# Optimization experiments

Hardware: AMD Instinct MI355X
Metric: run time of the kernel (lower is better)

The kernel has to match this reference:

```python
import jax, jax.numpy as jnp
import numpy as np

B, N, ND, H = 8, 1024, 64, 128
NUM_OPS, NUM_PARAMS, SKETCH = 64, 256, 128


def setup_inputs() -> dict:
    key = jax.random.key(0)
    ks = iter(jax.random.split(key, 64))

    def rn(shape, s=0.05):
        return jax.random.normal(next(ks), shape, dtype=jnp.float32) * s

    inp = {
        'node_features': jax.random.normal(next(ks), (B, N, ND), dtype=jnp.float32),
        'adjacency': (jax.random.uniform(next(ks), (B, N, N)) < 0.05).astype(jnp.float32),
        'mask': jnp.ones((B, N), jnp.float32),
    }
    for name, din in (('g1', ND), ('g2', H), ('g3', H)):
        inp[name + '_W'] = rn((din, H))
        inp[name + '_b'] = jnp.zeros((H,), jnp.float32)
        inp[name + '_aW'] = rn((2 * H,))
        inp[name + '_ab'] = jnp.zeros((), jnp.float32)
    for l in (0, 1):
        inp[f'l{l}_Wih'] = rn((4 * H, H))
        inp[f'l{l}_Whh'] = rn((4 * H, H))
        inp[f'l{l}_bih'] = jnp.zeros((4 * H,), jnp.float32)
        inp[f'l{l}_bhh'] = jnp.zeros((4 * H,), jnp.float32)
    for name, dout in (('op', NUM_OPS), ('pa', NUM_PARAMS), ('sk', SKETCH), ('no', ND)):
        inp[name + '_W1'] = rn((H, H))
        inp[name + '_b1'] = jnp.zeros((H,), jnp.float32)
        inp[name + '_W2'] = rn((H, dout))
        inp[name + '_b2'] = jnp.zeros((dout,), jnp.float32)
    return inp


def _gnn(x, adj, W, b, aW, ab):
    # h = Linear(x); att[b,i,j] = sigmoid(aW . [h_j ; h_i] + ab)  (cat order from the torch code)
    h = x @ W + b                      # [B,N,H]
    D = W.shape[1]
    sj = h @ aW[:D]                    # contribution of the dim-1-expanded term (h_j)
    si = h @ aW[D:]                    # contribution of the dim-2-expanded term (h_i)
    att = jax.nn.sigmoid(si[:, :, None] + sj[:, None, :] + ab) * adj  # [B,N,N]
    return jnp.einsum('bij,bjd->bid', att, h)


def _lstm(x, Wih, Whh, bih, bhh):
    # single torch-style LSTM layer, gate order i,f,g,o; zero initial state
    Bx, Hh = x.shape[0], Whh.shape[1]

    def step(carry, xt):
        h, c = carry
        g = xt @ Wih.T + h @ Whh.T + (bih + bhh)       # [B,4H]
        i, f, gg, o = jnp.split(g, 4, axis=-1)
        c = jax.nn.sigmoid(f) * c + jax.nn.sigmoid(i) * jnp.tanh(gg)
        h = jax.nn.sigmoid(o) * jnp.tanh(c)
        return (h, c), h

    z = jnp.zeros((Bx, Hh), x.dtype)
    _, ys = jax.lax.scan(step, (z, z), jnp.swapaxes(x, 0, 1))
    return jnp.swapaxes(ys, 0, 1)


def _mlp(x, W1, b1, W2, b2):
    return jax.nn.relu(x @ W1 + b1) @ W2 + b2


def reference(node_features, adjacency, mask,
              g1_W, g1_b, g1_aW, g1_ab,
              g2_W, g2_b, g2_aW, g2_ab,
              g3_W, g3_b, g3_aW, g3_ab,
              l0_Wih, l0_Whh, l0_bih, l0_bhh,
              l1_Wih, l1_Whh, l1_bih, l1_bhh,
              op_W1, op_b1, op_W2, op_b2,
              pa_W1, pa_b1, pa_W2, pa_b2,
              sk_W1, sk_b1, sk_W2, sk_b2,
              no_W1, no_b1, no_W2, no_b2):
    h = jax.nn.relu(_gnn(node_features, adjacency, g1_W, g1_b, g1_aW, g1_ab))
    h = jax.nn.relu(_gnn(h, adjacency, g2_W, g2_b, g2_aW, g2_ab))
    h = _gnn(h, adjacency, g3_W, g3_b, g3_aW, g3_ab)
    lo = _lstm(h, l0_Wih, l0_Whh, l0_bih, l0_bhh)
    lo = _lstm(lo, l1_Wih, l1_Whh, l1_bih, l1_bhh)
    op_pred = _mlp(lo, op_W1, op_b1, op_W2, op_b2)
    param_pred = _mlp(lo, pa_W1, pa_b1, pa_W2, pa_b2)
    sketch_pred = _mlp(lo, sk_W1, sk_b1, sk_W2, sk_b2)
    node_pred = _mlp(h, no_W1, no_b1, no_W2, no_b2)
    return (op_pred, param_pred, sketch_pred, node_pred)
```

## Files before the change

### kernel.cpp

```cpp
#include <hip/hip_runtime.h>

typedef __attribute__((ext_vector_type(8))) short short8;
typedef __attribute__((ext_vector_type(4))) float f32x4;
typedef __attribute__((ext_vector_type(2))) float f32x2;
typedef __attribute__((ext_vector_type(4))) unsigned short us4;
typedef __attribute__((ext_vector_type(2))) unsigned int u32x2;

__device__ __forceinline__ unsigned short bf16_of(float f) {
    unsigned u = __builtin_bit_cast(unsigned, f);
    u += 0x7fffu + ((u >> 16) & 1u);
    return (unsigned short)(u >> 16);
}
__device__ __forceinline__ unsigned bf16pk(float a, float b) {
    return (unsigned)bf16_of(a) | ((unsigned)bf16_of(b) << 16);
}
__device__ __forceinline__ float fexp2(float x) { return __builtin_amdgcn_exp2f(x); }
__device__ __forceinline__ float frcp(float x) { return __builtin_amdgcn_rcpf(x); }
__device__ __forceinline__ float sigm(float x) { return frcp(1.f + fexp2(-1.44269504f * x)); }
__device__ __forceinline__ float tanh_f(float x) {
    float e = fexp2(2.88539008f * x);
    return 1.f - 2.f * frcp(e + 1.f);
}
__device__ __forceinline__ f32x4 mfma16(short8 a, short8 b, f32x4 c) {
    return __builtin_amdgcn_mfma_f32_16x16x32_bf16(a, b, c, 0, 0, 0);
}
__device__ __forceinline__ float dpp_shr8(float x) {
    return __builtin_bit_cast(float, __builtin_amdgcn_update_dpp(
        0, __builtin_bit_cast(int, x), 0x118, 0xF, 0xF, true));
}
__device__ __forceinline__ float dpp_shl8(float x) {
    return __builtin_bit_cast(float, __builtin_amdgcn_update_dpp(
        0, __builtin_bit_cast(int, x), 0x108, 0xF, 0xF, true));
}

__global__ __launch_bounds__(256) void gemm_f32(
    const float* __restrict__ A, const float* __restrict__ B,
    const float* __restrict__ bias, float* __restrict__ C,
    int M, int N, int K, int BT, int RELU, int PACK)
{
    __shared__ float As[64][33];
    __shared__ float Bs[32][68];
    const int tid = threadIdx.x;
    const int tx = tid & 15, ty = tid >> 4;
    const int m0 = blockIdx.y * 64, n0 = blockIdx.x * 64;
    float acc[4][4];
#pragma unroll
    for (int i = 0; i < 4; ++i)
#pragma unroll
        for (int j = 0; j < 4; ++j) acc[i][j] = 0.f;

    for (int k0 = 0; k0 < K; k0 += 32) {
        __syncthreads();
        {
            const int r = tid >> 2, kk = (tid & 3) * 8;
            const float* src = A + (size_t)(m0 + r) * K + k0 + kk;
            f32x4 v0 = *(const f32x4*)src;
            f32x4 v1 = *(const f32x4*)(src + 4);
#pragma unroll
            for (int e = 0; e < 4; ++e) { As[r][kk + e] = v0[e]; As[r][kk + 4 + e] = v1[e]; }
        }
        if (!BT) {
            const int kk = tid >> 3, nn = (tid & 7) * 8;
            const float* src = B + (size_t)(k0 + kk) * N + n0 + nn;
            f32x4 v0 = *(const f32x4*)src;
            f32x4 v1 = *(const f32x4*)(src + 4);
#pragma unroll
            for (int e = 0; e < 4; ++e) { Bs[kk][nn + e] = v0[e]; Bs[kk][nn + 4 + e] = v1[e]; }
        } else {
            const int n = tid >> 2, kk = (tid & 3) * 8;
            const float* src = B + (size_t)(n0 + n) * K + k0 + kk;
            f32x4 v0 = *(const f32x4*)src;
            f32x4 v1 = *(const f32x4*)(src + 4);
#pragma unroll
            for (int e = 0; e < 4; ++e) { Bs[kk + e][n] = v0[e]; Bs[kk + 4 + e][n] = v1[e]; }
        }
        __syncthreads();
#pragma unroll 8
        for (int k = 0; k < 32; ++k) {
            float a0 = As[ty * 4 + 0][k], a1 = As[ty * 4 + 1][k];
            float a2 = As[ty * 4 + 2][k], a3 = As[ty * 4 + 3][k];
            f32x4 bv = *(const f32x4*)&Bs[k][tx * 4];
#pragma unroll
            for (int j = 0; j < 4; ++j) {
                acc[0][j] += a0 * bv[j]; acc[1][j] += a1 * bv[j];
                acc[2][j] += a2 * bv[j]; acc[3][j] += a3 * bv[j];
            }
        }
    }
    f32x4 bv = {};
    if (bias != nullptr) bv = *(const f32x4*)&bias[n0 + tx * 4];
#pragma unroll
    for (int i = 0; i < 4; ++i) {
        f32x4 res = {};
#pragma unroll
        for (int j = 0; j < 4; ++j) {
            float v = acc[i][j] + bv[j];
            if (RELU) v = fmaxf(v, 0.f);
            res[j] = v;
        }
        const int m = m0 + ty * 4 + i;
        if (!PACK) {
            *(f32x4*)&C[(size_t)m * N + n0 + tx * 4] = res;
        } else {
            const int b = m >> 10, t = m & 1023;
            const int n = n0 + tx * 4;
            const int pr = n >> 7, h = n & 127;
            *(f32x4*)&C[(((size_t)t * 4 + pr) * 8 + b) * 128 + h] = res;
        }
    }
}

__global__ __launch_bounds__(256) void sisj_kernel(
    const float* __restrict__ h, const float* __restrict__ aW,
    float* __restrict__ si, float* __restrict__ sj)
{
    const int tid = threadIdx.x, lane = tid & 63, w = tid >> 6;
    const int row = blockIdx.x * 4 + w;
    f32x2 hv = *(const f32x2*)(h + (size_t)row * 128 + lane * 2);
    f32x2 w1 = *(const f32x2*)&aW[lane * 2];
    f32x2 w2 = *(const f32x2*)&aW[128 + lane * 2];
    float sjp = hv[0] * w1[0] + hv[1] * w1[1];
    float sip = hv[0] * w2[0] + hv[1] * w2[1];
#pragma unroll
    for (int o = 32; o > 0; o >>= 1) {
        sjp += __shfl_xor(sjp, o);
        sip += __shfl_xor(sip, o);
    }
    if (lane == 0) { si[row] = sip; sj[row] = sjp; }
}

__global__ __launch_bounds__(256) void transpose_bf16_k(
    const float* __restrict__ h, unsigned short* __restrict__ hT)
{
    __shared__ float t[64][65];
    const int b = blockIdx.z, jt = blockIdx.x, dt = blockIdx.y;
    const int tid = threadIdx.x;
    const int r = tid >> 4, c4 = (tid & 15) * 4;
#pragma unroll
    for (int rr = 0; rr < 4; ++rr) {
        const int j = rr * 16 + r;
        f32x4 v = *(const f32x4*)(h + ((size_t)b * 1024 + jt * 64 + j) * 128 + dt * 64 + c4);
#pragma unroll
        for (int e = 0; e < 4; ++e) t[j][c4 + e] = v[e];
    }
    __syncthreads();
#pragma unroll
    for (int rr = 0; rr < 4; ++rr) {
        const int d = rr * 16 + r;
        u32x2 o;
        o[0] = bf16pk(t[c4 + 0][d], t[c4 + 1][d]);
        o[1] = bf16pk(t[c4 + 2][d], t[c4 + 3][d]);
        *(u32x2*)(hT + ((size_t)b * 128 + dt * 64 + d) * 1024 + jt * 64 + c4) = o;
    }
}

__global__ __launch_bounds__(256) void gnn_agg(
    const float* __restrict__ adj, const unsigned short* __restrict__ hT,
    const float* __restrict__ si, const float* __restrict__ sj,
    const float* __restrict__ abp, float* __restrict__ out, int RELU)
{
    __shared__ __align__(16) unsigned short Alds[64 * 40];
    __shared__ __align__(16) unsigned short Blds[128 * 40];
    const int b = blockIdx.y, it = blockIdx.x;
    const int i0 = it * 64;
    const int tid = threadIdx.x, lane = tid & 63, w = tid >> 6;
    const int quad = lane >> 4, col = lane & 15;
    const float ab = abp[0];
    const float* adjb = adj + (size_t)b * 1024 * 1024;
    const unsigned short* hTb = hT + (size_t)b * 128 * 1024;
    const float* sjb = sj + b * 1024;

    f32x4 acc[8] = {};
    const int ar_ = tid >> 2, ash = (tid & 3) * 8;
    const int br_ = tid >> 1, bsh = (tid & 1) * 16;
    const float sii = si[b * 1024 + i0 + ar_] + ab;

    for (int j0 = 0; j0 < 1024; j0 += 32) {
        __syncthreads();
        {
            const float* ar = adjb + (size_t)(i0 + ar_) * 1024 + j0 + ash;
            f32x4 av0 = *(const f32x4*)ar;
            f32x4 av1 = *(const f32x4*)(ar + 4);
            float s[8];
#pragma unroll
            for (int e = 0; e < 4; ++e) {
                s[e]     = sigm(sii + sjb[j0 + ash + e])     * av0[e];
                s[4 + e] = sigm(sii + sjb[j0 + ash + 4 + e]) * av1[e];
            }
            u32x2 o0 = {bf16pk(s[0], s[1]), bf16pk(s[2], s[3])};
            u32x2 o1 = {bf16pk(s[4], s[5]), bf16pk(s[6], s[7])};
            unsigned short* al = Alds + ar_ * 40 + ash;
            *(u32x2*)&al[0] = o0;
            *(u32x2*)&al[4] = o1;
        }
        {
            const unsigned short* bsrc = hTb + (size_t)br_ * 1024 + j0 + bsh;
            unsigned short* bl = Blds + br_ * 40 + bsh;
            *(short8*)&bl[0] = *(const short8*)&bsrc[0];
            *(short8*)&bl[8] = *(const short8*)&bsrc[8];
        }
        __syncthreads();
        short8 af = *(const short8*)&Alds[(w * 16 + col) * 40 + quad * 8];
#pragma unroll
        for (int nt = 0; nt < 8; ++nt) {
            short8 bf = *(const short8*)&Blds[(nt * 16 + col) * 40 + quad * 8];
            acc[nt] = mfma16(af, bf, acc[nt]);
        }
    }
    const int ibase = i0 + w * 16 + quad * 4;
#pragma unroll
    for (int nt = 0; nt < 8; ++nt) {
        const int d = nt * 16 + col;
#pragma unroll
        for (int r = 0; r < 4; ++r) {
            float v = acc[nt][r];
            if (RELU) v = fmaxf(v, 0.f);
            out[((size_t)b * 1024 + ibase + r) * 128 + d] = v;
        }
    }
}

struct PrepArgs {
    const float* src[8];
    unsigned short* dst[8];
    int N[8];
};
__global__ __launch_bounds__(256) void prep_k(
    PrepArgs pa, const float* bih0, const float* bhh0,
    float* bsum, int* flags)
{
    const int m = blockIdx.x;
    const int tid = threadIdx.x;
    if (m < 8) {
        const float* src = pa.src[m];
        unsigned short* dst = pa.dst[m];
        const int N = pa.N[m];
        const int n0 = tid >> 4, kc = (tid & 15) * 8;
        for (int n = n0; n < N; n += 16) {
            unsigned o[4];
#pragma unroll
            for (int e = 0; e < 8; e += 2)
                o[e >> 1] = bf16pk(src[(size_t)(kc + e) * N + n],
                                   src[(size_t)(kc + e + 1) * N + n]);
            *(u32x2*)&dst[n * 128 + kc] = *(u32x2*)&o[0];
            *(u32x2*)&dst[n * 128 + kc + 4] = *(u32x2*)&o[2];
        }
    } else {
        bsum[tid] = bih0[tid] + bhh0[tid];
        bsum[tid + 256] = bih0[tid + 256] + bhh0[tid + 256];
        if (tid < 3) flags[tid] = 0;
    }
}


struct HeadArgs {
    const unsigned short* W1T[4];
    const float* b1[4];
    const unsigned short* W2T[4];
    const float* b2[4];
    float* outp[4];
};

__device__ __forceinline__ void lstm_epilogue(
    const f32x4 accs[4], f32x4 xv0, f32x4 xv1, float* cst, float* hv, bool lo)
{
    float t0[4], t1[4];
#pragma unroll
    for (int i = 0; i < 4; ++i) {
        float P0 = 0.5f * ((lo ? accs[0][i] : dpp_shr8(accs[1][i])) + xv0[i]);
        float P1r = (lo ? accs[2][i] : dpp_shr8(accs[3][i])) + xv1[i];
        float P1 = lo ? P1r : 0.5f * P1r;
        t0[i] = tanh_f(P0);
        t1[i] = tanh_f(P1);
    }
    float c2[4], og[4];
#pragma unroll
    for (int i = 0; i < 4; ++i) {
        float ig = 0.5f + 0.5f * t0[i];
        float fg = 0.5f + 0.5f * dpp_shl8(t0[i]);
        float gg = t1[i];
        og[i] = 0.5f + 0.5f * dpp_shl8(t1[i]);
        c2[i] = fg * cst[i] + ig * gg;
        cst[i] = c2[i];
    }
    float pc0 = lo ? c2[0] : dpp_shr8(c2[1]);
    float pc1 = lo ? c2[2] : dpp_shr8(c2[3]);
    float tc0 = tanh_f(pc0), tc1 = tanh_f(pc1);
    float th[4] = {tc0, dpp_shl8(tc0), tc1, dpp_shl8(tc1)};
#pragma unroll
    for (int i = 0; i < 4; ++i) hv[i] = og[i] * th[i];
}

template <int SINK>
__device__ __forceinline__ void lstm_step(
    unsigned short* Hc, unsigned short* Hn, const short8 afr[4][4],
    f32x4 xv0, f32x4 xv1, float* cst, unsigned short* __restrict__ sink,
    int t, int col, int quad, int h4, int b)
{
    short8 bfr[4];
#pragma unroll
    for (int c = 0; c < 4; ++c)
        bfr[c] = *(const short8*)&Hc[col * 136 + c * 32 + quad * 8];
    f32x4 accs[4] = {};
#pragma unroll
    for (int c = 0; c < 4; ++c)
#pragma unroll
        for (int g = 0; g < 4; ++g)
            accs[g] = mfma16(afr[g][c], bfr[c], accs[g]);

    const bool lo = (col < 8);
    float hv[4];
    lstm_epilogue(accs, xv0, xv1, cst, hv, lo);
    if (lo) {
        u32x2 hb = {bf16pk(hv[0], hv[1]), bf16pk(hv[2], hv[3])};
        *(u32x2*)&Hn[b * 136 + h4] = hb;
        if (SINK == 0)
            *(u32x2*)(sink + (size_t)t * 1024 + b * 128 + h4) = hb;
        else
            *(u32x2*)(sink + ((size_t)t * 8 + b) * 128 + h4) = hb;
    }
    __builtin_amdgcn_s_waitcnt(0xC07F);
    __builtin_amdgcn_s_barrier();
}

template <int A32, int LROWS>
__device__ void head_strip(
    const void* __restrict__ Asrc, int row0,
    const unsigned short* __restrict__ W1T, const float* __restrict__ b1,
    const unsigned short* __restrict__ W2T, const float* __restrict__ b2,
    float* __restrict__ outp, int dout, unsigned short* A2, int tid)
{
    const int lane = tid & 63, w = tid >> 6;
    const int quad = lane >> 4, col = lane & 15;
    const int mrow = w * 16 + col;
    f32x4 acc[8] = {};
#pragma unroll
    for (int kc = 0; kc < 4; ++kc) {
        short8 af;
        if (A32) {
            const float* s = (const float*)Asrc + (size_t)(row0 + mrow) * 128 + kc * 32 + quad * 8;
            f32x4 v0 = *(const f32x4*)s, v1 = *(const f32x4*)(s + 4);
            short8 v;
#pragma unroll
            for (int j = 0; j < 4; ++j) {
                v[j] = (short)bf16_of(v0[j]);
                v[4 + j] = (short)bf16_of(v1[j]);
            }
            af = v;
        } else {
            af = *(const short8*)((const unsigned short*)Asrc +
                                  (size_t)(row0 + mrow) * 128 + kc * 32 + quad * 8);
        }
#pragma unroll
        for (int nt = 0; nt < 8; ++nt) {
            short8 bf = *(const short8*)&W1T[(nt * 16 + col) * 128 + kc * 32 + quad * 8];
            acc[nt] = mfma16(af, bf, acc[nt]);
        }
    }
    float b1v[8];
#pragma unroll
    for (int nt = 0; nt < 8; ++nt) b1v[nt] = b1[nt * 16 + col];
    __syncthreads();
#pragma unroll
    for (int nt = 0; nt < 8; ++nt)
#pragma unroll
        for (int i = 0; i < 4; ++i) {
            const int mm = w * 16 + quad * 4 + i;
            A2[mm * 136 + nt * 16 + col] = bf16_of(fmaxf(acc[nt][i] + b1v[nt], 0.f));
        }
    __syncthreads();
    const int ntiles = dout >> 4;
    for (int np = 0; np < ntiles; np += 8) {
        const int nts = (ntiles - np < 8) ? ntiles - np : 8;
        f32x4 acc2[8] = {};
#pragma unroll
        for (int kc = 0; kc < 4; ++kc) {
            short8 a2f = *(const short8*)&A2[mrow * 136 + kc * 32 + quad * 8];
            for (int nt = 0; nt < nts; ++nt) {
                short8 bf = *(const short8*)&W2T[((np + nt) * 16 + col) * 128 + kc * 32 + quad * 8];
                acc2[nt] = mfma16(a2f, bf, acc2[nt]);
            }
        }
        for (int nt = 0; nt < nts; ++nt) {
            const int n = (np + nt) * 16 + col;
            const float bb = b2[n];
#pragma unroll
            for (int i = 0; i < 4; ++i) {
                const int r = row0 + w * 16 + quad * 4 + i;
                size_t off;
                if (LROWS) off = ((size_t)(r & 7) * 1024 + (r >> 3)) * dout + n;
                else       off = (size_t)r * dout + n;
                outp[off] = acc2[nt][i] + bb;
            }
        }
    }
}

__global__ __launch_bounds__(512) void lstm_pipe(
    const float* __restrict__ xw0, const float* __restrict__ Whh0,
    const float* __restrict__ Wih1, const float* __restrict__ Whh1,
    const float* __restrict__ bih1, const float* __restrict__ bhh1,
    unsigned short* __restrict__ hbuf, float* __restrict__ xw1,
    int* __restrict__ flags, unsigned short* __restrict__ out1b,
    const float* __restrict__ bufH3, HeadArgs ha)
{
    __shared__ __align__(16) unsigned short H[2][16 * 136];
    __shared__ __align__(16) unsigned short A2[128 * 136];
    const int tid = threadIdx.x;
    const int lane = tid & 63;
    const int w = tid >> 6;
    const int quad = lane >> 4;
    const int col = lane & 15;
    const int b = col & 7;
    const int prA = col >> 3;
    const int h4 = w * 16 + quad * 4;

    if (blockIdx.x >= 3) {
        const int wid = blockIdx.x - 3;
        for (int s = wid; s < 64; s += 8)
            head_strip<1, 0>(bufH3, s * 128, ha.W1T[3], ha.b1[3],
                             ha.W2T[3], ha.b2[3], ha.outp[3], 64, A2, tid);
        for (int s = wid; s < 64; s += 8) {
            if (tid == 0) {
                while (__hip_atomic_load(&flags[2], __ATOMIC_ACQUIRE,
                                         __HIP_MEMORY_SCOPE_AGENT) < s + 1)
                    __builtin_amdgcn_s_sleep(16);
            }
            __syncthreads();
            head_strip<0, 1>(out1b, s * 128, ha.W1T[0], ha.b1[0],
                             ha.W2T[0], ha.b2[0], ha.outp[0], 64, A2, tid);
            head_strip<0, 1>(out1b, s * 128, ha.W1T[1], ha.b1[1],
                             ha.W2T[1], ha.b2[1], ha.outp[1], 256, A2, tid);
            head_strip<0, 1>(out1b, s * 128, ha.W1T[2], ha.b1[2],
                             ha.W2T[2], ha.b2[2], ha.outp[2], 128, A2, tid);
        }
        return;
    }

    if (blockIdx.x == 1) {
        short8 afrI[4][4];
        f32x4 biasv[4];
#pragma unroll
        for (int g = 0; g < 4; ++g) {
            const int row = g * 128 + w * 16 + col;
#pragma unroll
            for (int c = 0; c < 4; ++c) {
                const float* src = Wih1 + row * 128 + c * 32 + quad * 8;
                short8 v;
#pragma unroll
                for (int j = 0; j < 8; ++j) v[j] = (short)bf16_of(src[j]);
                afrI[g][c] = v;
            }
            const int rb = g * 128 + w * 16 + quad * 4;
            f32x4 b1 = *(const f32x4*)&bih1[rb];
            f32x4 b2 = *(const f32x4*)&bhh1[rb];
#pragma unroll
            for (int e = 0; e < 4; ++e) biasv[g][e] = b1[e] + b2[e];
        }
        for (int k = 0; k < 64; ++k) {
            if (tid == 0) {
                while (__hip_atomic_load(&flags[0], __ATOMIC_ACQUIRE,
                                         __HIP_MEMORY_SCOPE_AGENT) < k + 1)
                    __builtin_amdgcn_s_sleep(2);
                if (k >= 4) {
                    while (__hip_atomic_load(&flags[2], __ATOMIC_RELAXED,
                                             __HIP_MEMORY_SCOPE_AGENT) < k - 3)
                        __builtin_amdgcn_s_sleep(2);
                }
            }
            __builtin_amdgcn_s_waitcnt(0xC07F);
            __builtin_amdgcn_s_barrier();
            const unsigned short* hb = hbuf + (size_t)k * 16 * 1024;
            float* dst = xw1 + (size_t)(k & 3) * 65536;
#pragma unroll 2
            for (int nt = 0; nt < 8; ++nt) {
                const int tl = nt * 2 + (col >> 3);
                const unsigned short* src = hb + tl * 1024 + b * 128 + quad * 8;
                short8 bfr[4];
#pragma unroll
                for (int c = 0; c < 4; ++c) bfr[c] = *(const short8*)&src[c * 32];
                f32x4 acc[4] = {};
#pragma unroll
                for (int c = 0; c < 4; ++c)
#pragma unroll
                    for (int g = 0; g < 4; ++g)
                        acc[g] = mfma16(afrI[g][c], bfr[c], acc[g]);
#pragma unroll
                for (int g = 0; g < 4; ++g) {
                    f32x4 res;
#pragma unroll
                    for (int e = 0; e < 4; ++e) res[e] = acc[g][e] + biasv[g][e];
                    *(f32x4*)&dst[((tl * 4 + g) * 8 + b) * 128 + w * 16 + quad * 4] = res;
                }
            }
            __builtin_amdgcn_s_waitcnt(0x0F70);
            __builtin_amdgcn_s_barrier();
            if (tid == 0)
                __hip_atomic_store(&flags[1], k + 1, __ATOMIC_RELEASE,
                                   __HIP_MEMORY_SCOPE_AGENT);
        }
        return;
    }

    for (int i = tid; i < 2 * 16 * 136; i += 512) (&H[0][0])[i] = 0;
    float cst[4] = {0.f, 0.f, 0.f, 0.f};
    const int lane_off = (prA * 8 + b) * 128 + h4;

    if (blockIdx.x == 0) {
        short8 afr[4][4];
#pragma unroll
        for (int g = 0; g < 4; ++g) {
            const int row = g * 128 + w * 16 + col;
#pragma unroll
            for (int c = 0; c < 4; ++c) {
                const float* src = Whh0 + row * 128 + c * 32 + quad * 8;
                short8 v;
#pragma unroll
                for (int j = 0; j < 8; ++j) v[j] = (short)bf16_of(src[j]);
                afr[g][c] = v;
            }
        }
        const float* xp = xw0 + lane_off;
        f32x4 p0a = *(const f32x4*)(xp);
        f32x4 p1a = *(const f32x4*)(xp + 2048);
        f32x4 p0b = *(const f32x4*)(xp + 4096);
        f32x4 p1b = *(const f32x4*)(xp + 6144);
        xp += 8192;
        __syncthreads();

        for (int t = 0; t < 1024; t += 2) {
            const float* xr = (t == 1022) ? xp - 8192 : xp;
            {
                f32x4 xv0 = p0a, xv1 = p1a;
                p0a = *(const f32x4*)(xr);
                p1a = *(const f32x4*)(xr + 2048);
                lstm_step<0>(&H[0][0], &H[1][0], afr, xv0, xv1, cst, hbuf, t, col, quad, h4, b);
            }
            {
                f32x4 xv0 = p0b, xv1 = p1b;
                p0b = *(const f32x4*)(xr + 4096);
                p1b = *(const f32x4*)(xr + 6144);
                lstm_step<0>(&H[1][0], &H[0][0], afr, xv0, xv1, cst, hbuf, t + 1, col, quad, h4, b);
            }
            xp += 8192;
            if ((t & 14) == 14) {
                __syncthreads();
                if (tid == 0)
                    __hip_atomic_store(&flags[0], (t >> 4) + 1, __ATOMIC_RELEASE,
                                       __HIP_MEMORY_SCOPE_AGENT);
            }
        }
    } else {
        short8 afr[4][4];
#pragma unroll
        for (int g = 0; g < 4; ++g) {
            const int row = g * 128 + w * 16 + col;
#pragma unroll
            for (int c = 0; c < 4; ++c) {
                const float* src = Whh1 + row * 128 + c * 32 + quad * 8;
                short8 v;
#pragma unroll
                for (int j = 0; j < 8; ++j) v[j] = (short)bf16_of(src[j]);
                afr[g][c] = v;
            }
        }
        __syncthreads();
        auto xaddr = [&](int t) -> const float* {
            return xw1 + (((t >> 4) & 3) * 65536 + (t & 15) * 4096) + lane_off;
        };
        while (__hip_atomic_load(&flags[1], __ATOMIC_ACQUIRE,
                                 __HIP_MEMORY_SCOPE_AGENT) < 2)
            __builtin_amdgcn_s_sleep(2);
        f32x4 p0a = *(const f32x4*)xaddr(0);
        f32x4 p1a = *(const f32x4*)(xaddr(0) + 2048);
        f32x4 p0b = *(const f32x4*)xaddr(1);
        f32x4 p1b = *(const f32x4*)(xaddr(1) + 2048);

        for (int c = 0; c < 64; ++c) {
            if (c > 0) {
                const int target = (c + 2 < 64) ? c + 2 : 64;
                if (tid == 0) {
                    while (__hip_atomic_load(&flags[1], __ATOMIC_ACQUIRE,
                                             __HIP_MEMORY_SCOPE_AGENT) < target)
                        __builtin_amdgcn_s_sleep(2);
                }
                __builtin_amdgcn_s_waitcnt(0xC07F);
                __builtin_amdgcn_s_barrier();
            }
            for (int s = 0; s < 16; s += 2) {
                const int t = c * 16 + s;
                const int t2 = (t + 2 < 1024) ? t + 2 : 1023;
                const int t3 = (t + 3 < 1024) ? t + 3 : 1023;
                {
                    f32x4 xv0 = p0a, xv1 = p1a;
                    p0a = *(const f32x4*)xaddr(t2);
                    p1a = *(const f32x4*)(xaddr(t2) + 2048);
                    lstm_step<1>(&H[0][0], &H[1][0], afr, xv0, xv1, cst, out1b, t, col, quad, h4, b);
                }
                {
                    f32x4 xv0 = p0b, xv1 = p1b;
                    p0b = *(const f32x4*)xaddr(t3);
                    p1b = *(const f32x4*)(xaddr(t3) + 2048);
                    lstm_step<1>(&H[1][0], &H[0][0], afr, xv0, xv1, cst, out1b, t + 1, col, quad, h4, b);
                }
            }
            __syncthreads();
            if (tid == 0)
                __hip_atomic_store(&flags[2], c + 1, __ATOMIC_RELEASE,
                                   __HIP_MEMORY_SCOPE_AGENT);
        }
    }
}

extern "C" void kernel_launch(void* const* d_in, const int* in_sizes, int n_in,
                              void* d_out, int out_size, void* d_ws, size_t ws_size,
                              hipStream_t stream)
{
    (void)in_sizes; (void)n_in; (void)out_size; (void)ws_size;
    const float* nf    = (const float*)d_in[0];
    const float* adj   = (const float*)d_in[1];
    const float* g1W   = (const float*)d_in[3];
    const float* g1b   = (const float*)d_in[4];
    const float* g1aW  = (const float*)d_in[5];
    const float* g1ab  = (const float*)d_in[6];
    const float* g2W   = (const float*)d_in[7];
    const float* g2b   = (const float*)d_in[8];
    const float* g2aW  = (const float*)d_in[9];
    const float* g2ab  = (const float*)d_in[10];
    const float* g3W   = (const float*)d_in[11];
    const float* g3b   = (const float*)d_in[12];
    const float* g3aW  = (const float*)d_in[13];
    const float* g3ab  = (const float*)d_in[14];
    const float* l0Wih = (const float*)d_in[15];
    const float* l0Whh = (const float*)d_in[16];
    const float* l0bih = (const float*)d_in[17];
    const float* l0bhh = (const float*)d_in[18];
    const float* l1Wih = (const float*)d_in[19];
    const float* l1Whh = (const float*)d_in[20];
    const float* l1bih = (const float*)d_in[21];
    const float* l1bhh = (const float*)d_in[22];
    const float* opW1 = (const float*)d_in[23];
    const float* opb1 = (const float*)d_in[24];
    const float* opW2 = (const float*)d_in[25];
    const float* opb2 = (const float*)d_in[26];
    const float* paW1 = (const float*)d_in[27];
    const float* pab1 = (const float*)d_in[28];
    const float* paW2 = (const float*)d_in[29];
    const float* pab2 = (const float*)d_in[30];
    const float* skW1 = (const float*)d_in[31];
    const float* skb1 = (const float*)d_in[32];
    const float* skW2 = (const float*)d_in[33];
    const float* skb2 = (const float*)d_in[34];
    const float* noW1 = (const float*)d_in[35];
    const float* nob1 = (const float*)d_in[36];
    const float* noW2 = (const float*)d_in[37];
    const float* nob2 = (const float*)d_in[38];

    float* out = (float*)d_out;
    float* ws = (float*)d_ws;
    float* bufH  = ws;
    float* bufX  = ws + 1048576;
    float* bufH3 = ws + 2097152;
    unsigned short* bufT = (unsigned short*)(ws + 3145728);
    float* siB  = ws + 3670016;
    float* sjB  = ws + 3678208;
    float* bsum = ws + 3686400;
    float* xw0  = ws + 3687424;
    float* xw1  = ws + 7881728;
    int*  flags = (int*)(ws + 8143872);
    unsigned short* WT = (unsigned short*)(ws + 8143876);
    unsigned short* out1b = (unsigned short*)(ws + 8209412);
    unsigned short* hbuf = (unsigned short*)bufX;

    unsigned short* opW1T = WT;
    unsigned short* paW1T = WT + 16384;
    unsigned short* skW1T = WT + 32768;
    unsigned short* noW1T = WT + 49152;
    unsigned short* opW2T = WT + 65536;
    unsigned short* paW2T = WT + 73728;
    unsigned short* skW2T = WT + 106496;
    unsigned short* noW2T = WT + 122880;

    auto gemm = [&](const float* A, const float* B, const float* bias, float* C,
                    int M, int N, int K, int BT, int RELU, int PACK = 0) {
        dim3 g(N / 64, M / 64);
        gemm_f32<<<g, dim3(256), 0, stream>>>(A, B, bias, C, M, N, K, BT, RELU, PACK);
    };

    gemm(nf, g1W, g1b, bufH, 8192, 128, 64, 0, 0);
    sisj_kernel<<<2048, 256, 0, stream>>>(bufH, g1aW, siB, sjB);
    transpose_bf16_k<<<dim3(16, 2, 8), 256, 0, stream>>>(bufH, bufT);
    gnn_agg<<<dim3(16, 8), 256, 0, stream>>>(adj, bufT, siB, sjB, g1ab, bufX, 1);
    gemm(bufX, g2W, g2b, bufH, 8192, 128, 128, 0, 0);
    sisj_kernel<<<2048, 256, 0, stream>>>(bufH, g2aW, siB, sjB);
    transpose_bf16_k<<<dim3(16, 2, 8), 256, 0, stream>>>(bufH, bufT);
    gnn_agg<<<dim3(16, 8), 256, 0, stream>>>(adj, bufT, siB, sjB, g2ab, bufX, 1);
    gemm(bufX, g3W, g3b, bufH, 8192, 128, 128, 0, 0);
    sisj_kernel<<<2048, 256, 0, stream>>>(bufH, g3aW, siB, sjB);
    transpose_bf16_k<<<dim3(16, 2, 8), 256, 0, stream>>>(bufH, bufT);
    gnn_agg<<<dim3(16, 8), 256, 0, stream>>>(adj, bufT, siB, sjB, g3ab, bufH3, 0);

    PrepArgs pargs;
    pargs.src[0] = opW1; pargs.dst[0] = opW1T; pargs.N[0] = 128;
    pargs.src[1] = paW1; pargs.dst[1] = paW1T; pargs.N[1] = 128;
    pargs.src[2] = skW1; pargs.dst[2] = skW1T; pargs.N[2] = 128;
    pargs.src[3] = noW1; pargs.dst[3] = noW1T; pargs.N[3] = 128;
    pargs.src[4] = opW2; pargs.dst[4] = opW2T; pargs.N[4] = 64;
    pargs.src[5] = paW2; pargs.dst[5] = paW2T; pargs.N[5] = 256;
    pargs.src[6] = skW2; pargs.dst[6] = skW2T; pargs.N[6] = 128;
    pargs.src[7] = noW2; pargs.dst[7] = noW2T; pargs.N[7] = 64;
    prep_k<<<9, 256, 0, stream>>>(pargs, l0bih, l0bhh, bsum, flags);

    gemm(bufH3, l0Wih, bsum, xw0, 8192, 512, 128, 1, 0, 1);

    HeadArgs ha;
    ha.W1T[0] = opW1T; ha.b1[0] = opb1; ha.W2T[0] = opW2T; ha.b2[0] = opb2;
    ha.outp[0] = out + 0;
    ha.W1T[1] = paW1T; ha.b1[1] = pab1; ha.W2T[1] = paW2T; ha.b2[1] = pab2;
    ha.outp[1] = out + 524288;
    ha.W1T[2] = skW1T; ha.b1[2] = skb1; ha.W2T[2] = skW2T; ha.b2[2] = skb2;
    ha.outp[2] = out + 2621440;
    ha.W1T[3] = noW1T; ha.b1[3] = nob1; ha.W2T[3] = noW2T; ha.b2[3] = nob2;
    ha.outp[3] = out + 3670016;
    lstm_pipe<<<11, 512, 0, stream>>>(xw0, l0Whh, l1Wih, l1Whh, l1bih, l1bhh,
                                      hbuf, xw1, flags, out1b, bufH3, ha);
}
```

Before: 1.401 ms.

## Fuse layer-0 LSTM input projection into pipelined persistent kernel and merge GNN aux kernels

The separate fp32 GEMM that computed the layer-0 LSTM input projection is removed. A new producer block inside lstm_pipe now computes it chunk by chunk with bf16 MFMA and signals progress through a flag, so the recurrent layer-0 block can start once the first chunks are ready instead of waiting for the whole GEMM. The sisj and transpose kernels are merged into one aux kernel that reads each tile of h once, and weight prep (now also converting Wih0 to bf16) moves before the GNN. The cost is reduced input-projection precision and a possible stall of the recurrence on the producer block if it falls behind.

```diff
diff --git a/kernel.cpp b/kernel.cpp
--- a/kernel.cpp
+++ b/kernel.cpp
@@ -36,7 +36,7 @@
 __global__ __launch_bounds__(256) void gemm_f32(
     const float* __restrict__ A, const float* __restrict__ B,
     const float* __restrict__ bias, float* __restrict__ C,
-    int M, int N, int K, int BT, int RELU, int PACK)
+    int M, int N, int K, int RELU)
 {
     __shared__ float As[64][33];
     __shared__ float Bs[32][68];
@@ -59,20 +59,13 @@
 #pragma unroll
             for (int e = 0; e < 4; ++e) { As[r][kk + e] = v0[e]; As[r][kk + 4 + e] = v1[e]; }
         }
-        if (!BT) {
+        {
             const int kk = tid >> 3, nn = (tid & 7) * 8;
             const float* src = B + (size_t)(k0 + kk) * N + n0 + nn;
             f32x4 v0 = *(const f32x4*)src;
             f32x4 v1 = *(const f32x4*)(src + 4);
 #pragma unroll
             for (int e = 0; e < 4; ++e) { Bs[kk][nn + e] = v0[e]; Bs[kk][nn + 4 + e] = v1[e]; }
-        } else {
-            const int n = tid >> 2, kk = (tid & 3) * 8;
-            const float* src = B + (size_t)(n0 + n) * K + k0 + kk;
-            f32x4 v0 = *(const f32x4*)src;
-            f32x4 v1 = *(const f32x4*)(src + 4);
-#pragma unroll
-            for (int e = 0; e < 4; ++e) { Bs[kk + e][n] = v0[e]; Bs[kk + 4 + e][n] = v1[e]; }
         }
         __syncthreads();
 #pragma unroll 8
@@ -87,8 +80,7 @@
             }
         }
     }
-    f32x4 bv = {};
-    if (bias != nullptr) bv = *(const f32x4*)&bias[n0 + tx * 4];
+    f32x4 bv = *(const f32x4*)&bias[n0 + tx * 4];
 #pragma unroll
     for (int i = 0; i < 4; ++i) {
         f32x4 res = {};
@@ -98,59 +90,49 @@
             if (RELU) v = fmaxf(v, 0.f);
             res[j] = v;
         }
-        const int m = m0 + ty * 4 + i;
-        if (!PACK) {
-            *(f32x4*)&C[(size_t)m * N + n0 + tx * 4] = res;
-        } else {
-            const int b = m >> 10, t = m & 1023;
-            const int n = n0 + tx * 4;
-            const int pr = n >> 7, h = n & 127;
-            *(f32x4*)&C[(((size_t)t * 4 + pr) * 8 + b) * 128 + h] = res;
-        }
-    }
-}
-
-__global__ __launch_bounds__(256) void sisj_kernel(
+        *(f32x4*)&C[(size_t)(m0 + ty * 4 + i) * N + n0 + tx * 4] = res;
+    }
+}
+
+__global__ __launch_bounds__(256) void aux_k(
     const float* __restrict__ h, const float* __restrict__ aW,
-    float* __restrict__ si, float* __restrict__ sj)
-{
-    const int tid = threadIdx.x, lane = tid & 63, w = tid >> 6;
-    const int row = blockIdx.x * 4 + w;
-    f32x2 hv = *(const f32x2*)(h + (size_t)row * 128 + lane * 2);
-    f32x2 w1 = *(const f32x2*)&aW[lane * 2];
-    f32x2 w2 = *(const f32x2*)&aW[128 + lane * 2];
-    float sjp = hv[0] * w1[0] + hv[1] * w1[1];
-    float sip = hv[0] * w2[0] + hv[1] * w2[1];
-#pragma unroll
-    for (int o = 32; o > 0; o >>= 1) {
-        sjp += __shfl_xor(sjp, o);
-        sip += __shfl_xor(sip, o);
-    }
-    if (lane == 0) { si[row] = sip; sj[row] = sjp; }
-}
-
-__global__ __launch_bounds__(256) void transpose_bf16_k(
-    const float* __restrict__ h, unsigned short* __restrict__ hT)
-{
-    __shared__ float t[64][65];
-    const int b = blockIdx.z, jt = blockIdx.x, dt = blockIdx.y;
+    float* __restrict__ si, float* __restrict__ sj,
+    unsigned short* __restrict__ hT)
+{
+    __shared__ float t[64][129];
+    __shared__ float awl[256];
+    const int jt = blockIdx.x, b = blockIdx.y;
     const int tid = threadIdx.x;
-    const int r = tid >> 4, c4 = (tid & 15) * 4;
-#pragma unroll
-    for (int rr = 0; rr < 4; ++rr) {
-        const int j = rr * 16 + r;
-        f32x4 v = *(const f32x4*)(h + ((size_t)b * 1024 + jt * 64 + j) * 128 + dt * 64 + c4);
-#pragma unroll
-        for (int e = 0; e < 4; ++e) t[j][c4 + e] = v[e];
+    awl[tid] = aW[tid];
+    {
+        const int r = tid >> 2, c8 = (tid & 3) * 32;
+        const float* src = h + ((size_t)b * 1024 + jt * 64 + r) * 128 + c8;
+#pragma unroll
+        for (int e = 0; e < 32; e += 4)
+            *(f32x4*)&t[r][c8 + e] = *(const f32x4*)(src + e);
     }
     __syncthreads();
-#pragma unroll
-    for (int rr = 0; rr < 4; ++rr) {
-        const int d = rr * 16 + r;
-        u32x2 o;
-        o[0] = bf16pk(t[c4 + 0][d], t[c4 + 1][d]);
-        o[1] = bf16pk(t[c4 + 2][d], t[c4 + 3][d]);
-        *(u32x2*)(hT + ((size_t)b * 128 + dt * 64 + d) * 1024 + jt * 64 + c4) = o;
+    if (tid < 64) {
+        float sjp = 0.f, sip = 0.f;
+#pragma unroll 8
+        for (int d = 0; d < 128; ++d) {
+            float v = t[tid][d];
+            sjp += v * awl[d];
+            sip += v * awl[128 + d];
+        }
+        si[b * 1024 + jt * 64 + tid] = sip;
+        sj[b * 1024 + jt * 64 + tid] = sjp;
+    }
+    {
+        const int d = tid >> 1, j0 = (tid & 1) * 32;
+        unsigned short* dst = hT + ((size_t)b * 128 + d) * 1024 + jt * 64 + j0;
+#pragma unroll
+        for (int j = 0; j < 32; j += 4) {
+            u32x2 o;
+            o[0] = bf16pk(t[j0 + j][d], t[j0 + j + 1][d]);
+            o[1] = bf16pk(t[j0 + j + 2][d], t[j0 + j + 3][d]);
+            *(u32x2*)(dst + j) = o;
+        }
     }
 }
 
@@ -226,8 +208,8 @@
     int N[8];
 };
 __global__ __launch_bounds__(256) void prep_k(
-    PrepArgs pa, const float* bih0, const float* bhh0,
-    float* bsum, int* flags)
+    PrepArgs pa, const float* __restrict__ Wih0,
+    unsigned short* __restrict__ Wih0T, int* flags)
 {
     const int m = blockIdx.x;
     const int tid = threadIdx.x;
@@ -246,9 +228,16 @@
             *(u32x2*)&dst[n * 128 + kc + 4] = *(u32x2*)&o[2];
         }
     } else {
-        bsum[tid] = bih0[tid] + bhh0[tid];
-        bsum[tid + 256] = bih0[tid + 256] + bhh0[tid + 256];
-        if (tid < 3) flags[tid] = 0;
+        if (m == 8 && tid < 8) flags[tid] = 0;
+        const int base = (m - 8) * 32768;
+        for (int i = base + tid * 8; i < base + 32768; i += 2048) {
+            f32x4 v0 = *(const f32x4*)&Wih0[i];
+            f32x4 v1 = *(const f32x4*)&Wih0[i + 4];
+            u32x2 o = {bf16pk(v0[0], v0[1]), bf16pk(v0[2], v0[3])};
+            u32x2 o2 = {bf16pk(v1[0], v1[1]), bf16pk(v1[2], v1[3])};
+            *(u32x2*)&Wih0T[i] = o;
+            *(u32x2*)&Wih0T[i + 4] = o2;
+        }
     }
 }
 
@@ -397,7 +386,9 @@
 }
 
 __global__ __launch_bounds__(512) void lstm_pipe(
-    const float* __restrict__ xw0, const float* __restrict__ Whh0,
+    float* __restrict__ xw0, const unsigned short* __restrict__ Wih0T,
+    const float* __restrict__ bih0, const float* __restrict__ bhh0,
+    const float* __restrict__ Whh0,
     const float* __restrict__ Wih1, const float* __restrict__ Whh1,
     const float* __restrict__ bih1, const float* __restrict__ bhh1,
     unsigned short* __restrict__ hbuf, float* __restrict__ xw1,
@@ -415,8 +406,8 @@
     const int prA = col >> 3;
     const int h4 = w * 16 + quad * 4;
 
-    if (blockIdx.x >= 3) {
-        const int wid = blockIdx.x - 3;
+    if (blockIdx.x >= 4) {
+        const int wid = blockIdx.x - 4;
         for (int s = wid; s < 64; s += 8)
             head_strip<1, 0>(bufH3, s * 128, ha.W1T[3], ha.b1[3],
                              ha.W2T[3], ha.b2[3], ha.outp[3], 64, A2, tid);
@@ -433,6 +424,56 @@
                              ha.W2T[1], ha.b2[1], ha.outp[1], 256, A2, tid);
             head_strip<0, 1>(out1b, s * 128, ha.W1T[2], ha.b1[2],
                              ha.W2T[2], ha.b2[2], ha.outp[2], 128, A2, tid);
+        }
+        return;
+    }
+
+    if (blockIdx.x == 3) {
+        float biasv[32];
+#pragma unroll
+        for (int nt = 0; nt < 32; ++nt) {
+            const int n = nt * 16 + col;
+            biasv[nt] = bih0[n] + bhh0[n];
+        }
+        const int rr = w * 16 + col;
+        const int tl = rr >> 3, bb = rr & 7;
+        for (int c = 0; c < 64; ++c) {
+            short8 af[4];
+            const float* as = bufH3 + ((size_t)bb * 1024 + c * 16 + tl) * 128;
+#pragma unroll
+            for (int kc = 0; kc < 4; ++kc) {
+                f32x4 v0 = *(const f32x4*)(as + kc * 32 + quad * 8);
+                f32x4 v1 = *(const f32x4*)(as + kc * 32 + quad * 8 + 4);
+                short8 v;
+#pragma unroll
+                for (int j = 0; j < 4; ++j) {
+                    v[j] = (short)bf16_of(v0[j]);
+                    v[4 + j] = (short)bf16_of(v1[j]);
+                }
+                af[kc] = v;
+            }
+#pragma unroll 4
+            for (int nt = 0; nt < 32; ++nt) {
+                f32x4 acc = {};
+#pragma unroll
+                for (int kc = 0; kc < 4; ++kc) {
+                    short8 bf = *(const short8*)&Wih0T[(nt * 16 + col) * 128 + kc * 32 + quad * 8];
+                    acc = mfma16(af[kc], bf, acc);
+                }
+                const int n = nt * 16 + col;
+                const int pr = n >> 7, hh = n & 127;
+#pragma unroll
+                for (int i = 0; i < 4; ++i) {
+                    const int r2 = w * 16 + quad * 4 + i;
+                    const int tl2 = r2 >> 3, bb2 = r2 & 7;
+                    xw0[(((size_t)(c * 16 + tl2) * 4 + pr) * 8 + bb2) * 128 + hh]
+                        = acc[i] + biasv[nt];
+                }
+            }
+            __syncthreads();
+            if (tid == 0)
+                __hip_atomic_store(&flags[3], c + 1, __ATOMIC_RELEASE,
+                                   __HIP_MEMORY_SCOPE_AGENT);
         }
         return;
     }
@@ -520,35 +561,50 @@
                 afr[g][c] = v;
             }
         }
-        const float* xp = xw0 + lane_off;
-        f32x4 p0a = *(const f32x4*)(xp);
-        f32x4 p1a = *(const f32x4*)(xp + 2048);
-        f32x4 p0b = *(const f32x4*)(xp + 4096);
-        f32x4 p1b = *(const f32x4*)(xp + 6144);
-        xp += 8192;
+        auto xaddr = [&](int t) -> const float* {
+            return xw0 + (size_t)t * 4096 + lane_off;
+        };
+        if (tid == 0) {
+            while (__hip_atomic_load(&flags[3], __ATOMIC_ACQUIRE,
+                                     __HIP_MEMORY_SCOPE_AGENT) < 1)
+                __builtin_amdgcn_s_sleep(2);
+        }
         __syncthreads();
-
-        for (int t = 0; t < 1024; t += 2) {
-            const float* xr = (t == 1022) ? xp - 8192 : xp;
-            {
-                f32x4 xv0 = p0a, xv1 = p1a;
-                p0a = *(const f32x4*)(xr);
-                p1a = *(const f32x4*)(xr + 2048);
-                lstm_step<0>(&H[0][0], &H[1][0], afr, xv0, xv1, cst, hbuf, t, col, quad, h4, b);
-            }
-            {
-                f32x4 xv0 = p0b, xv1 = p1b;
-                p0b = *(const f32x4*)(xr + 4096);
-                p1b = *(const f32x4*)(xr + 6144);
-                lstm_step<0>(&H[1][0], &H[0][0], afr, xv0, xv1, cst, hbuf, t + 1, col, quad, h4, b);
-            }
-            xp += 8192;
-            if ((t & 14) == 14) {
-                __syncthreads();
-                if (tid == 0)
-                    __hip_atomic_store(&flags[0], (t >> 4) + 1, __ATOMIC_RELEASE,
-                                       __HIP_MEMORY_SCOPE_AGENT);
-            }
+        f32x4 p0a = *(const f32x4*)xaddr(0);
+        f32x4 p1a = *(const f32x4*)(xaddr(0) + 2048);
+        f32x4 p0b = *(const f32x4*)xaddr(1);
+        f32x4 p1b = *(const f32x4*)(xaddr(1) + 2048);
+
+        for (int c = 0; c < 64; ++c) {
+            const int need = (c + 2 < 64) ? c + 2 : 64;
+            if (tid == 0) {
+                while (__hip_atomic_load(&flags[3], __ATOMIC_ACQUIRE,
+                                         __HIP_MEMORY_SCOPE_AGENT) < need)
+                    __builtin_amdgcn_s_sleep(2);
+            }
+            __builtin_amdgcn_s_waitcnt(0xC07F);
+            __builtin_amdgcn_s_barrier();
+            for (int s = 0; s < 16; s += 2) {
+                const int t = c * 16 + s;
+                const int t2 = (t + 2 < 1024) ? t + 2 : 1023;
+                const int t3 = (t + 3 < 1024) ? t + 3 : 1023;
+                {
+                    f32x4 xv0 = p0a, xv1 = p1a;
+                    p0a = *(const f32x4*)xaddr(t2);
+                    p1a = *(const f32x4*)(xaddr(t2) + 2048);
+                    lstm_step<0>(&H[0][0], &H[1][0], afr, xv0, xv1, cst, hbuf, t, col, quad, h4, b);
+                }
+                {
+                    f32x4 xv0 = p0b, xv1 = p1b;
+                    p0b = *(const f32x4*)xaddr(t3);
+                    p1b = *(const f32x4*)(xaddr(t3) + 2048);
+                    lstm_step<0>(&H[1][0], &H[0][0], afr, xv0, xv1, cst, hbuf, t + 1, col, quad, h4, b);
+                }
+            }
+            __syncthreads();
+            if (tid == 0)
+                __hip_atomic_store(&flags[0], c + 1, __ATOMIC_RELEASE,
+                                   __HIP_MEMORY_SCOPE_AGENT);
         }
     } else {
         short8 afr[4][4];
@@ -664,12 +720,12 @@
     unsigned short* bufT = (unsigned short*)(ws + 3145728);
     float* siB  = ws + 3670016;
     float* sjB  = ws + 3678208;
-    float* bsum = ws + 3686400;
-    float* xw0  = ws + 3687424;
-    float* xw1  = ws + 7881728;
-    int*  flags = (int*)(ws + 8143872);
-    unsigned short* WT = (unsigned short*)(ws + 8143876);
-    unsigned short* out1b = (unsigned short*)(ws + 8209412);
+    float* xw0  = ws + 3686400;
+    float* xw1  = ws + 7880704;
+    int*  flags = (int*)(ws + 8142848);
+    unsigned short* WT = (unsigned short*)(ws + 8142864);
+    unsigned short* Wih0T = (unsigned short*)(ws + 8208400);
+    unsigned short* out1b = (unsigned short*)(ws + 8241168);
     unsigned short* hbuf = (unsigned short*)bufX;
 
     unsigned short* opW1T = WT;
@@ -682,23 +738,10 @@
     unsigned short* noW2T = WT + 122880;
 
     auto gemm = [&](const float* A, const float* B, const float* bias, float* C,
-                    int M, int N, int K, int BT, int RELU, int PACK = 0) {
+                    int M, int N, int K, int RELU) {
         dim3 g(N / 64, M / 64);
-        gemm_f32<<<g, dim3(256), 0, stream>>>(A, B, bias, C, M, N, K, BT, RELU, PACK);
+        gemm_f32<<<g, dim3(256), 0, stream>>>(A, B, bias, C, M, N, K, RELU);
     };
-
-    gemm(nf, g1W, g1b, bufH, 8192, 128, 64, 0, 0);
-    sisj_kernel<<<2048, 256, 0, stream>>>(bufH, g1aW, siB, sjB);
-    transpose_bf16_k<<<dim3(16, 2, 8), 256, 0, stream>>>(bufH, bufT);
-    gnn_agg<<<dim3(16, 8), 256, 0, stream>>>(adj, bufT, siB, sjB, g1ab, bufX, 1);
-    gemm(bufX, g2W, g2b, bufH, 8192, 128, 128, 0, 0);
-    sisj_kernel<<<2048, 256, 0, stream>>>(bufH, g2aW, siB, sjB);
-    transpose_bf16_k<<<dim3(16, 2, 8), 256, 0, stream>>>(bufH, bufT);
-    gnn_agg<<<dim3(16, 8), 256, 0, stream>>>(adj, bufT, siB, sjB, g2ab, bufX, 1);
-    gemm(bufX, g3W, g3b, bufH, 8192, 128, 128, 0, 0);
-    sisj_kernel<<<2048, 256, 0, stream>>>(bufH, g3aW, siB, sjB);
-    transpose_bf16_k<<<dim3(16, 2, 8), 256, 0, stream>>>(bufH, bufT);
-    gnn_agg<<<dim3(16, 8), 256, 0, stream>>>(adj, bufT, siB, sjB, g3ab, bufH3, 0);
 
     PrepArgs pargs;
     pargs.src[0] = opW1; pargs.dst[0] = opW1T; pargs.N[0] = 128;
@@ -709,9 +752,17 @@
     pargs.src[5] = paW2; pargs.dst[5] = paW2T; pargs.N[5] = 256;
     pargs.src[6] = skW2; pargs.dst[6] = skW2T; pargs.N[6] = 128;
     pargs.src[7] = noW2; pargs.dst[7] = noW2T; pargs.N[7] = 64;
-    prep_k<<<9, 256, 0, stream>>>(pargs, l0bih, l0bhh, bsum, flags);
-
-    gemm(bufH3, l0Wih, bsum, xw0, 8192, 512, 128, 1, 0, 1);
+    prep_k<<<10, 256, 0, stream>>>(pargs, l0Wih, Wih0T, flags);
+
+    gemm(nf, g1W, g1b, bufH, 8192, 128, 64, 0);
+    aux_k<<<dim3(16, 8), 256, 0, stream>>>(bufH, g1aW, siB, sjB, bufT);
+    gnn_agg<<<dim3(16, 8), 256, 0, stream>>>(adj, bufT, siB, sjB, g1ab, bufX, 1);
+    gemm(bufX, g2W, g2b, bufH, 8192, 128, 128, 0);
+    aux_k<<<dim3(16, 8), 256, 0, stream>>>(bufH, g2aW, siB, sjB, bufT);
+    gnn_agg<<<dim3(16, 8), 256, 0, stream>>>(adj, bufT, siB, sjB, g2ab, bufX, 1);
+    gemm(bufX, g3W, g3b, bufH, 8192, 128, 128, 0);
+    aux_k<<<dim3(16, 8), 256, 0, stream>>>(bufH, g3aW, siB, sjB, bufT);
+    gnn_agg<<<dim3(16, 8), 256, 0, stream>>>(adj, bufT, siB, sjB, g3ab, bufH3, 0);
 
     HeadArgs ha;
     ha.W1T[0] = opW1T; ha.b1[0] = opb1; ha.W2T[0] = opW2T; ha.b2[0] = opb2;
@@ -722,6 +773,7 @@
     ha.outp[2] = out + 2621440;
     ha.W1T[3] = noW1T; ha.b1[3] = nob1; ha.W2T[3] = noW2T; ha.b2[3] = nob2;
     ha.outp[3] = out + 3670016;
-    lstm_pipe<<<11, 512, 0, stream>>>(xw0, l0Whh, l1Wih, l1Whh, l1bih, l1bhh,
+    lstm_pipe<<<12, 512, 0, stream>>>(xw0, Wih0T, l0bih, l0bhh, l0Whh,
+                                      l1Wih, l1Whh, l1bih, l1bhh,
                                       hbuf, xw1, flags, out1b, bufH3, ha);
 }
```

Result: slower. 2.500 ms (+78.4%).
